# Kernel optimization log

Measured on AMD Instinct MI355X. Metric: run time of the kernel, lower is better.

## Reference

```python
import jax, jax.numpy as jnp
import numpy as np

B, NUM_GENES, F = 8, 20000, 128
N, E, H = 50000, 800000, 128


def setup_inputs() -> dict:
    key = jax.random.key(0)
    k = jax.random.split(key, 8)
    gene_emb = jax.random.normal(k[0], (B, NUM_GENES, F), dtype=jnp.float32)
    W1 = jax.random.normal(k[1], (F, H), dtype=jnp.float32) * 0.05
    b1 = jnp.zeros((H,), dtype=jnp.float32)
    W2 = jax.random.normal(k[2], (H, H), dtype=jnp.float32) * 0.05
    b2 = jnp.zeros((H,), dtype=jnp.float32)
    global_ids = jax.random.randint(k[3], (N,), 0, NUM_GENES, dtype=jnp.int64)
    edge_index = jax.random.randint(k[4], (2, E), 0, N, dtype=jnp.int64)
    return {"gene_emb": gene_emb, "W1": W1, "b1": b1, "W2": W2, "b2": b2,
            "global_ids": global_ids, "edge_index": edge_index}


def reference(gene_emb, W1, b1, W2, b2, global_ids, edge_index):
    n = global_ids.shape[0]
    # GCN normalization with self-loops (PyG GCNConv default):
    # A_hat = A + I, deg over target nodes, norm = d^{-1/2}[src] * d^{-1/2}[dst]
    loop = jnp.arange(n)
    src = jnp.concatenate([edge_index[0], loop])  # [E+N]
    dst = jnp.concatenate([edge_index[1], loop])  # [E+N]
    deg = jnp.zeros((n,), gene_emb.dtype).at[dst].add(1.0)
    dinv = jax.lax.rsqrt(deg)  # deg >= 1 thanks to self-loops
    norm = (dinv[src] * dinv[dst])[None, :, None]  # [1, E+N, 1]

    def gcn(x, W, b):
        h = x @ W                                   # [B, N, H] transform first (linear commutes)
        msg = h[:, src, :] * norm                   # gather + scale: [B, E+N, H]
        agg = jnp.zeros_like(h).at[:, dst].add(msg)  # scatter-add over targets
        return agg + b

    x = gene_emb[:, global_ids, :]                  # [B, N, F] node feature gather
    x = jax.nn.relu(gcn(x, W1, b1))
    x = gcn(x, W2, b2)
    # global_mean_pool: each batch replica is one whole graph -> mean over nodes
    return x.mean(axis=1)                           # [B, H]
```

## Files before the change

kernel.cpp:

```cpp
#include <hip/hip_runtime.h>

#define NG 20000
#define BB 8
#define FD 128

typedef unsigned int uint;
typedef unsigned short ushort;
typedef __attribute__((ext_vector_type(8))) short short8v;
typedef __attribute__((ext_vector_type(4))) float float4v;


__global__ void k_init(float* deg, float* s_acc, int N) {
    int i = blockIdx.x * blockDim.x + threadIdx.x;
    if (i < N) deg[i] = 1.0f;
    if (i < BB * FD) s_acc[i] = 0.0f;
}

__global__ void k_zero(int4* p, int n4) {
    int i = blockIdx.x * blockDim.x + threadIdx.x;
    if (i < n4) p[i] = make_int4(0, 0, 0, 0);
}

__global__ void k_count(const int* __restrict__ dst, float* deg, int E) {
    int e = blockIdx.x * blockDim.x + threadIdx.x;
    if (e < E) atomicAdd(&deg[dst[e]], 1.0f);
}

__global__ void k_node(const float* __restrict__ deg, float* dinv, float* cval,
                       float* wself, int* padcnt, int N) {
    int i = blockIdx.x * blockDim.x + threadIdx.x;
    if (i < N) {
        float d = deg[i];
        dinv[i]  = rsqrtf(d);
        float iv = 1.0f / d;
        cval[i]  = iv;
        wself[i] = iv;
        int nv = (int)d;
        padcnt[i] = (nv + 7) & ~7;
    }
}

__global__ void k_scan1(const int* __restrict__ padcnt, int* offs, int* bsums, int N) {
    __shared__ int sd[256];
    int t = threadIdx.x, idx = blockIdx.x * 256 + t;
    int v = (idx < N) ? padcnt[idx] : 0;
    sd[t] = v; __syncthreads();
    for (int o = 1; o < 256; o <<= 1) {
        int x = (t >= o) ? sd[t - o] : 0;
        __syncthreads();
        sd[t] += x;
        __syncthreads();
    }
    if (idx < N) offs[idx] = sd[t] - v;
    if (t == 255) bsums[blockIdx.x] = sd[255];
}

__global__ void k_scan2(int* bsums, int nb) {
    __shared__ int sd[256];
    int t = threadIdx.x;
    int v = (t < nb) ? bsums[t] : 0;
    sd[t] = v; __syncthreads();
    for (int o = 1; o < 256; o <<= 1) {
        int x = (t >= o) ? sd[t - o] : 0;
        __syncthreads();
        sd[t] += x;
        __syncthreads();
    }
    if (t < nb) bsums[t] = sd[t] - v;
}

__global__ void k_scan3(int* offs, const int* __restrict__ bsums, int N) {
    int i = blockIdx.x * blockDim.x + threadIdx.x;
    if (i < N) offs[i] += bsums[blockIdx.x];
}

__global__ void k_self(const int* __restrict__ gid, const float* __restrict__ wself,
                       const int* __restrict__ offs, int* cursor, int2* csr, int N) {
    int i = blockIdx.x * blockDim.x + threadIdx.x;
    if (i < N) {
        csr[offs[i]] = make_int2(gid[i], __float_as_int(wself[i]));
        cursor[i] = 1;
    }
}

__global__ void k_fill(const int* __restrict__ src, const int* __restrict__ dst,
                       const int* __restrict__ gid, const float* __restrict__ dinv,
                       float* cval, const int* __restrict__ offs, int* cursor,
                       int2* csr, int E) {
    int e = blockIdx.x * blockDim.x + threadIdx.x;
    if (e >= E) return;
    int s = src[e], d = dst[e];
    float nrm = dinv[s] * dinv[d];
    atomicAdd(&cval[s], nrm);
    int pos = atomicAdd(&cursor[d], 1);
    csr[offs[d] + pos] = make_int2(gid[s], __float_as_int(nrm));
}

__device__ __forceinline__ ushort f2bf(float x) {
    uint u = __float_as_uint(x);
    u += 0x7FFFu + ((u >> 16) & 1u);
    return (ushort)(u >> 16);
}
__device__ __forceinline__ float bf_lo(uint u) { return __uint_as_float(u << 16); }
__device__ __forceinline__ float bf_hi(uint u) { return __uint_as_float(u & 0xFFFF0000u); }

__global__ void k_w1t(const float* __restrict__ W1, ushort* __restrict__ w1t) {
    int j = blockIdx.x, k = threadIdx.x;
    w1t[j * 128 + k] = f2bf(W1[k * 128 + j]);
}

__global__ __launch_bounds__(256, 3)
void k_h(const float* __restrict__ gene, const ushort* __restrict__ w1t,
         ushort* __restrict__ h2) {
    __shared__ ushort Al[64 * 128];
    __shared__ ushort Bl[128 * 128];
    int t = threadIdx.x;
    size_t row0 = (size_t)blockIdx.x * 64;

#pragma unroll
    for (int s = 0; s < 8; s++) {
        int f = t + s * 256;
        int r = f >> 5, k0 = (f & 31) * 4;
        float4 v = *(const float4*)(gene + (row0 + r) * 128 + k0);
        ushort4 u;
        u.x = f2bf(v.x); u.y = f2bf(v.y); u.z = f2bf(v.z); u.w = f2bf(v.w);
        int byte = (r * 256 + k0 * 2) ^ ((r & 7) << 4);
        *(ushort4*)((char*)Al + byte) = u;
    }
#pragma unroll
    for (int s = 0; s < 8; s++) {
        int f = t + s * 256;
        int j = f >> 4, k0 = (f & 15) * 8;
        uint4 v = *(const uint4*)(w1t + j * 128 + k0);
        int byte = (j * 256 + k0 * 2) ^ ((j & 7) << 4);
        *(uint4*)((char*)Bl + byte) = v;
    }
    __syncthreads();

    int wid = t >> 6, lane = t & 63;
    int r0 = wid * 16;
    int lrow = lane & 15, lhi = lane >> 4;
    float4v acc[8];
#pragma unroll
    for (int nf = 0; nf < 8; nf++) acc[nf] = (float4v)(0.f);

#pragma unroll
    for (int c = 0; c < 4; c++) {
        int ra = r0 + lrow;
        int byteA = (ra * 256 + (c * 32 + lhi * 8) * 2) ^ ((ra & 7) << 4);
        short8v a = *(short8v*)((char*)Al + byteA);
#pragma unroll
        for (int nf = 0; nf < 8; nf++) {
            int jb = nf * 16 + lrow;
            int byteB = (jb * 256 + (c * 32 + lhi * 8) * 2) ^ ((jb & 7) << 4);
            short8v b = *(short8v*)((char*)Bl + byteB);
            acc[nf] = __builtin_amdgcn_mfma_f32_16x16x32_bf16(a, b, acc[nf], 0, 0, 0);
        }
    }
#pragma unroll
    for (int nf = 0; nf < 8; nf++) {
#pragma unroll
        for (int q = 0; q < 4; q++) {
            int rr = lhi * 4 + q;
            int cc = nf * 16 + lrow;
            h2[(row0 + r0 + rr) * 128 + cc] = f2bf(acc[nf][q]);
        }
    }
}

__global__ __launch_bounds__(512)
void k_aggs(const uint* __restrict__ hb, const int2* __restrict__ csr,
            const int* __restrict__ offs, const int* __restrict__ padcnt,
            const float* __restrict__ cval, const float* __restrict__ b1,
            float* __restrict__ s_acc, int N, int npw) {
    int b    = blockIdx.x & 7;
    int wid  = threadIdx.x >> 6, lane = threadIdx.x & 63;
    int w    = __builtin_amdgcn_readfirstlane((blockIdx.x >> 3) * 8 + wid);
    const uint* base = hb + (size_t)b * NG * 64;
    int j = lane * 2;
    float bx = b1[j], by = b1[j + 1];
    float sx = 0.f, sy = 0.f;

    int i0 = w * npw;
    int i1 = min(N, i0 + npw);
    for (int i = i0; i < i1; ++i) {
        int   e  = offs[i];
        int   pc = padcnt[i];
        float cv = cval[i];
        float ax = 0.f, ay = 0.f;
        for (int q = 0; q < pc; q += 8) {
            int ee = e + q;
            int2 c0 = csr[ee],     c1 = csr[ee + 1], c2 = csr[ee + 2], c3 = csr[ee + 3];
            int2 c4 = csr[ee + 4], c5 = csr[ee + 5], c6 = csr[ee + 6], c7 = csr[ee + 7];
            uint u0 = base[(size_t)c0.x * 64 + lane];
            uint u1 = base[(size_t)c1.x * 64 + lane];
            uint u2 = base[(size_t)c2.x * 64 + lane];
            uint u3 = base[(size_t)c3.x * 64 + lane];
            uint u4 = base[(size_t)c4.x * 64 + lane];
            uint u5 = base[(size_t)c5.x * 64 + lane];
            uint u6 = base[(size_t)c6.x * 64 + lane];
            uint u7 = base[(size_t)c7.x * 64 + lane];
            float n0 = __int_as_float(c0.y), n1 = __int_as_float(c1.y);
            float n2 = __int_as_float(c2.y), n3 = __int_as_float(c3.y);
            float n4 = __int_as_float(c4.y), n5 = __int_as_float(c5.y);
            float n6 = __int_as_float(c6.y), n7 = __int_as_float(c7.y);
            ax = fmaf(n0, bf_lo(u0), ax); ay = fmaf(n0, bf_hi(u0), ay);
            ax = fmaf(n1, bf_lo(u1), ax); ay = fmaf(n1, bf_hi(u1), ay);
            ax = fmaf(n2, bf_lo(u2), ax); ay = fmaf(n2, bf_hi(u2), ay);
            ax = fmaf(n3, bf_lo(u3), ax); ay = fmaf(n3, bf_hi(u3), ay);
            ax = fmaf(n4, bf_lo(u4), ax); ay = fmaf(n4, bf_hi(u4), ay);
            ax = fmaf(n5, bf_lo(u5), ax); ay = fmaf(n5, bf_hi(u5), ay);
            ax = fmaf(n6, bf_lo(u6), ax); ay = fmaf(n6, bf_hi(u6), ay);
            ax = fmaf(n7, bf_lo(u7), ax); ay = fmaf(n7, bf_hi(u7), ay);
        }
        sx += cv * fmaxf(ax + bx, 0.f);
        sy += cv * fmaxf(ay + by, 0.f);
    }

    __shared__ float red[8][128];
    red[wid][j]     = sx;
    red[wid][j + 1] = sy;
    __syncthreads();
    int t = threadIdx.x;
    if (t < 128) {
        float s = 0.f;
#pragma unroll
        for (int wv = 0; wv < 8; wv++) s += red[wv][t];
        atomicAdd(&s_acc[b * 128 + t], s);
    }
}

__global__ void k_final(const float* __restrict__ s_acc, const float* __restrict__ W2,
                        const float* __restrict__ b2, float* __restrict__ out, float invN) {
    __shared__ float ss[1024];
    int t = threadIdx.x;
    for (int idx = t; idx < 1024; idx += 128) ss[idx] = s_acc[idx];
    __syncthreads();
    float acc[8];
#pragma unroll
    for (int b = 0; b < 8; b++) acc[b] = 0.f;
    for (int k = 0; k < 128; k++) {
        float w = W2[k * 128 + t];
#pragma unroll
        for (int b = 0; b < 8; b++) acc[b] += ss[b * 128 + k] * w;
    }
    float bb = b2[t];
#pragma unroll
    for (int b = 0; b < 8; b++) out[b * 128 + t] = acc[b] * invN + bb;
}


extern "C" void kernel_launch(void* const* d_in, const int* in_sizes, int n_in,
                              void* d_out, int out_size, void* d_ws, size_t ws_size,
                              hipStream_t stream) {
    const float* gene = (const float*)d_in[0];
    const float* W1   = (const float*)d_in[1];
    const float* b1   = (const float*)d_in[2];
    const float* W2   = (const float*)d_in[3];
    const float* b2   = (const float*)d_in[4];
    const int*   gid  = (const int*)d_in[5];
    const int*   eidx = (const int*)d_in[6];
    int N = in_sizes[5];
    int E = in_sizes[6] / 2;
    const int* src = eidx;
    const int* dst = eidx + E;
    float* out = (float*)d_out;

    char* p = (char*)d_ws;
    auto alloc = [&](size_t bytes) -> char* {
        char* r = p; p += (bytes + 255) & ~(size_t)255; return r;
    };
    size_t csr_cap = (size_t)E + 8 * (size_t)N;
    float* deg    = (float*)alloc((size_t)N * 4);
    float* dinv   = (float*)alloc((size_t)N * 4);
    float* cval   = (float*)alloc((size_t)N * 4);
    float* wself  = (float*)alloc((size_t)N * 4);
    int*   padcnt = (int*)  alloc((size_t)N * 4);
    int*   offs   = (int*)  alloc((size_t)N * 4);
    int*   cursor = (int*)  alloc((size_t)N * 4);
    int*   bsums  = (int*)  alloc(256 * 4);
    int2*  csr    = (int2*) alloc(csr_cap * 8);
    float* s_acc  = (float*)alloc(1024 * 4);
    ushort* h2    = (ushort*)alloc((size_t)NG * BB * FD * 2);
    ushort* w1t   = (ushort*)alloc(128 * 128 * 2);

    int nb = (N + 255) / 256;
    int eb = (E + 255) / 256;
    int zn4 = (int)(csr_cap * 8 / 16);
    int zb  = (zn4 + 255) / 256;

    const int NBLK = 2048;
    int wavesPerBatch = (NBLK / 8) * 8;
    int npw = (N + wavesPerBatch - 1) / wavesPerBatch;

    k_init <<<nb, 256, 0, stream>>>(deg, s_acc, N);
    k_zero <<<zb, 256, 0, stream>>>((int4*)csr, zn4);
    k_w1t  <<<128, 128, 0, stream>>>(W1, w1t);
    k_count<<<eb, 256, 0, stream>>>(dst, deg, E);
    k_node <<<nb, 256, 0, stream>>>(deg, dinv, cval, wself, padcnt, N);
    k_scan1<<<nb, 256, 0, stream>>>(padcnt, offs, bsums, N);
    k_scan2<<<1, 256, 0, stream>>>(bsums, nb);
    k_scan3<<<nb, 256, 0, stream>>>(offs, bsums, N);
    k_self <<<nb, 256, 0, stream>>>(gid, wself, offs, cursor, csr, N);
    k_fill <<<eb, 256, 0, stream>>>(src, dst, gid, dinv, cval, offs, cursor, csr, E);
    k_h    <<<(NG * BB) / 64, 256, 0, stream>>>(gene, w1t, h2);
    k_aggs <<<NBLK, 512, 0, stream>>>((const uint*)h2, csr, offs, padcnt,
                                      cval, b1, s_acc, N, npw);
    k_final<<<1, 128, 0, stream>>>(s_acc, W2, b2, out, 1.0f / (float)N);
}
```

Baseline: 332.7 us.

## Interleave batch pairs in the hidden layout and fuse setup/scan kernels

The bf16 hidden features are now stored with two batch replicas interleaved per feature. This lets the aggregation kernel gather 8 bytes per lane covering two batches at once, so each CSR edge read is shared across two batches and the number of CSR passes halves. Several small preprocessing kernels (init, zero, W1 transpose, node stats, scan stages, self-loop fill) are merged into fewer launches to cut launch overhead. Each wave now does twice the work per node and holds more accumulator registers.

```diff
diff --git a/kernel.cpp b/kernel.cpp
--- a/kernel.cpp
+++ b/kernel.cpp
@@ -9,16 +9,24 @@
 typedef __attribute__((ext_vector_type(8))) short short8v;
 typedef __attribute__((ext_vector_type(4))) float float4v;
 
-
-__global__ void k_init(float* deg, float* s_acc, int N) {
+__device__ __forceinline__ ushort f2bf(float x) {
+    uint u = __float_as_uint(x);
+    u += 0x7FFFu + ((u >> 16) & 1u);
+    return (ushort)(u >> 16);
+}
+__device__ __forceinline__ float bf_lo(uint u) { return __uint_as_float(u << 16); }
+__device__ __forceinline__ float bf_hi(uint u) { return __uint_as_float(u & 0xFFFF0000u); }
+
+__global__ void k_setup(int4* csrz, int zn4, float* deg, float* s_acc,
+                        const float* __restrict__ W1, ushort* w1t, int N) {
     int i = blockIdx.x * blockDim.x + threadIdx.x;
+    if (i < zn4) csrz[i] = make_int4(0, 0, 0, 0);
     if (i < N) deg[i] = 1.0f;
     if (i < BB * FD) s_acc[i] = 0.0f;
-}
-
-__global__ void k_zero(int4* p, int n4) {
-    int i = blockIdx.x * blockDim.x + threadIdx.x;
-    if (i < n4) p[i] = make_int4(0, 0, 0, 0);
+    if (i < FD * FD) {
+        int j = i >> 7, k = i & 127;
+        w1t[i] = f2bf(W1[k * 128 + j]);
+    }
 }
 
 __global__ void k_count(const int* __restrict__ dst, float* deg, int E) {
@@ -26,24 +34,20 @@
     if (e < E) atomicAdd(&deg[dst[e]], 1.0f);
 }
 
-__global__ void k_node(const float* __restrict__ deg, float* dinv, float* cval,
-                       float* wself, int* padcnt, int N) {
-    int i = blockIdx.x * blockDim.x + threadIdx.x;
-    if (i < N) {
-        float d = deg[i];
-        dinv[i]  = rsqrtf(d);
-        float iv = 1.0f / d;
-        cval[i]  = iv;
-        wself[i] = iv;
-        int nv = (int)d;
-        padcnt[i] = (nv + 7) & ~7;
-    }
-}
-
-__global__ void k_scan1(const int* __restrict__ padcnt, int* offs, int* bsums, int N) {
+__global__ void k_scanA(const float* __restrict__ deg, float* dinv, float* cval,
+                        float* wself, int* padcnt, int* offs, int* bsums, int N) {
     __shared__ int sd[256];
     int t = threadIdx.x, idx = blockIdx.x * 256 + t;
-    int v = (idx < N) ? padcnt[idx] : 0;
+    int v = 0;
+    if (idx < N) {
+        float d = deg[idx];
+        dinv[idx]  = rsqrtf(d);
+        float iv = 1.0f / d;
+        cval[idx]  = iv;
+        wself[idx] = iv;
+        v = ((int)d + 7) & ~7;
+        padcnt[idx] = v;
+    }
     sd[t] = v; __syncthreads();
     for (int o = 1; o < 256; o <<= 1) {
         int x = (t >= o) ? sd[t - o] : 0;
@@ -69,16 +73,14 @@
     if (t < nb) bsums[t] = sd[t] - v;
 }
 
-__global__ void k_scan3(int* offs, const int* __restrict__ bsums, int N) {
-    int i = blockIdx.x * blockDim.x + threadIdx.x;
-    if (i < N) offs[i] += bsums[blockIdx.x];
-}
-
-__global__ void k_self(const int* __restrict__ gid, const float* __restrict__ wself,
-                       const int* __restrict__ offs, int* cursor, int2* csr, int N) {
+__global__ void k_scanB(int* offs, const int* __restrict__ bsums,
+                        const int* __restrict__ gid, const float* __restrict__ wself,
+                        int* cursor, int2* csr, int N) {
     int i = blockIdx.x * blockDim.x + threadIdx.x;
     if (i < N) {
-        csr[offs[i]] = make_int2(gid[i], __float_as_int(wself[i]));
+        int o = offs[i] + bsums[blockIdx.x];
+        offs[i] = o;
+        csr[o] = make_int2(gid[i], __float_as_int(wself[i]));
         cursor[i] = 1;
     }
 }
@@ -96,19 +98,6 @@
     csr[offs[d] + pos] = make_int2(gid[s], __float_as_int(nrm));
 }
 
-__device__ __forceinline__ ushort f2bf(float x) {
-    uint u = __float_as_uint(x);
-    u += 0x7FFFu + ((u >> 16) & 1u);
-    return (ushort)(u >> 16);
-}
-__device__ __forceinline__ float bf_lo(uint u) { return __uint_as_float(u << 16); }
-__device__ __forceinline__ float bf_hi(uint u) { return __uint_as_float(u & 0xFFFF0000u); }
-
-__global__ void k_w1t(const float* __restrict__ W1, ushort* __restrict__ w1t) {
-    int j = blockIdx.x, k = threadIdx.x;
-    w1t[j * 128 + k] = f2bf(W1[k * 128 + j]);
-}
-
 __global__ __launch_bounds__(256, 3)
 void k_h(const float* __restrict__ gene, const ushort* __restrict__ w1t,
          ushort* __restrict__ h2) {
@@ -163,23 +152,27 @@
         for (int q = 0; q < 4; q++) {
             int rr = lhi * 4 + q;
             int cc = nf * 16 + lrow;
-            h2[(row0 + r0 + rr) * 128 + cc] = f2bf(acc[nf][q]);
+            int rGlob = (int)row0 + r0 + rr;
+            int bb = rGlob / NG;
+            int gg = rGlob - bb * NG;
+            size_t di = ((size_t)(bb >> 1) * NG + gg) * 256 + cc * 2 + (bb & 1);
+            h2[di] = f2bf(acc[nf][q]);
         }
     }
 }
 
 __global__ __launch_bounds__(512)
-void k_aggs(const uint* __restrict__ hb, const int2* __restrict__ csr,
+void k_aggp(const uint* __restrict__ hp, const int2* __restrict__ csr,
             const int* __restrict__ offs, const int* __restrict__ padcnt,
             const float* __restrict__ cval, const float* __restrict__ b1,
             float* __restrict__ s_acc, int N, int npw) {
-    int b    = blockIdx.x & 7;
+    int p    = blockIdx.x & 3;
     int wid  = threadIdx.x >> 6, lane = threadIdx.x & 63;
-    int w    = __builtin_amdgcn_readfirstlane((blockIdx.x >> 3) * 8 + wid);
-    const uint* base = hb + (size_t)b * NG * 64;
-    int j = lane * 2;
-    float bx = b1[j], by = b1[j + 1];
-    float sx = 0.f, sy = 0.f;
+    int w    = __builtin_amdgcn_readfirstlane((blockIdx.x >> 2) * 8 + wid);
+    const uint* bp = hp + (size_t)p * NG * 128 + lane * 2;
+    int l2 = lane * 2;
+    float bx = b1[l2], by = b1[l2 + 1];
+    float sx0 = 0.f, sx1 = 0.f, sy0 = 0.f, sy1 = 0.f;
 
     int i0 = w * npw;
     int i1 = min(N, i0 + npw);
@@ -187,46 +180,59 @@
         int   e  = offs[i];
         int   pc = padcnt[i];
         float cv = cval[i];
-        float ax = 0.f, ay = 0.f;
+        float ax0 = 0.f, ax1 = 0.f, ay0 = 0.f, ay1 = 0.f;
         for (int q = 0; q < pc; q += 8) {
             int ee = e + q;
             int2 c0 = csr[ee],     c1 = csr[ee + 1], c2 = csr[ee + 2], c3 = csr[ee + 3];
             int2 c4 = csr[ee + 4], c5 = csr[ee + 5], c6 = csr[ee + 6], c7 = csr[ee + 7];
-            uint u0 = base[(size_t)c0.x * 64 + lane];
-            uint u1 = base[(size_t)c1.x * 64 + lane];
-            uint u2 = base[(size_t)c2.x * 64 + lane];
-            uint u3 = base[(size_t)c3.x * 64 + lane];
-            uint u4 = base[(size_t)c4.x * 64 + lane];
-            uint u5 = base[(size_t)c5.x * 64 + lane];
-            uint u6 = base[(size_t)c6.x * 64 + lane];
-            uint u7 = base[(size_t)c7.x * 64 + lane];
+            uint2 u0 = *(const uint2*)(bp + (size_t)c0.x * 128);
+            uint2 u1 = *(const uint2*)(bp + (size_t)c1.x * 128);
+            uint2 u2 = *(const uint2*)(bp + (size_t)c2.x * 128);
+            uint2 u3 = *(const uint2*)(bp + (size_t)c3.x * 128);
+            uint2 u4 = *(const uint2*)(bp + (size_t)c4.x * 128);
+            uint2 u5 = *(const uint2*)(bp + (size_t)c5.x * 128);
+            uint2 u6 = *(const uint2*)(bp + (size_t)c6.x * 128);
+            uint2 u7 = *(const uint2*)(bp + (size_t)c7.x * 128);
             float n0 = __int_as_float(c0.y), n1 = __int_as_float(c1.y);
             float n2 = __int_as_float(c2.y), n3 = __int_as_float(c3.y);
             float n4 = __int_as_float(c4.y), n5 = __int_as_float(c5.y);
             float n6 = __int_as_float(c6.y), n7 = __int_as_float(c7.y);
-            ax = fmaf(n0, bf_lo(u0), ax); ay = fmaf(n0, bf_hi(u0), ay);
-            ax = fmaf(n1, bf_lo(u1), ax); ay = fmaf(n1, bf_hi(u1), ay);
-            ax = fmaf(n2, bf_lo(u2), ax); ay = fmaf(n2, bf_hi(u2), ay);
-            ax = fmaf(n3, bf_lo(u3), ax); ay = fmaf(n3, bf_hi(u3), ay);
-            ax = fmaf(n4, bf_lo(u4), ax); ay = fmaf(n4, bf_hi(u4), ay);
-            ax = fmaf(n5, bf_lo(u5), ax); ay = fmaf(n5, bf_hi(u5), ay);
-            ax = fmaf(n6, bf_lo(u6), ax); ay = fmaf(n6, bf_hi(u6), ay);
-            ax = fmaf(n7, bf_lo(u7), ax); ay = fmaf(n7, bf_hi(u7), ay);
+            ax0 = fmaf(n0, bf_lo(u0.x), ax0); ax1 = fmaf(n0, bf_hi(u0.x), ax1);
+            ay0 = fmaf(n0, bf_lo(u0.y), ay0); ay1 = fmaf(n0, bf_hi(u0.y), ay1);
+            ax0 = fmaf(n1, bf_lo(u1.x), ax0); ax1 = fmaf(n1, bf_hi(u1.x), ax1);
+            ay0 = fmaf(n1, bf_lo(u1.y), ay0); ay1 = fmaf(n1, bf_hi(u1.y), ay1);
+            ax0 = fmaf(n2, bf_lo(u2.x), ax0); ax1 = fmaf(n2, bf_hi(u2.x), ax1);
+            ay0 = fmaf(n2, bf_lo(u2.y), ay0); ay1 = fmaf(n2, bf_hi(u2.y), ay1);
+            ax0 = fmaf(n3, bf_lo(u3.x), ax0); ax1 = fmaf(n3, bf_hi(u3.x), ax1);
+            ay0 = fmaf(n3, bf_lo(u3.y), ay0); ay1 = fmaf(n3, bf_hi(u3.y), ay1);
+            ax0 = fmaf(n4, bf_lo(u4.x), ax0); ax1 = fmaf(n4, bf_hi(u4.x), ax1);
+            ay0 = fmaf(n4, bf_lo(u4.y), ay0); ay1 = fmaf(n4, bf_hi(u4.y), ay1);
+            ax0 = fmaf(n5, bf_lo(u5.x), ax0); ax1 = fmaf(n5, bf_hi(u5.x), ax1);
+            ay0 = fmaf(n5, bf_lo(u5.y), ay0); ay1 = fmaf(n5, bf_hi(u5.y), ay1);
+            ax0 = fmaf(n6, bf_lo(u6.x), ax0); ax1 = fmaf(n6, bf_hi(u6.x), ax1);
+            ay0 = fmaf(n6, bf_lo(u6.y), ay0); ay1 = fmaf(n6, bf_hi(u6.y), ay1);
+            ax0 = fmaf(n7, bf_lo(u7.x), ax0); ax1 = fmaf(n7, bf_hi(u7.x), ax1);
+            ay0 = fmaf(n7, bf_lo(u7.y), ay0); ay1 = fmaf(n7, bf_hi(u7.y), ay1);
         }
-        sx += cv * fmaxf(ax + bx, 0.f);
-        sy += cv * fmaxf(ay + by, 0.f);
-    }
-
-    __shared__ float red[8][128];
-    red[wid][j]     = sx;
-    red[wid][j + 1] = sy;
+        sx0 += cv * fmaxf(ax0 + bx, 0.f);
+        sx1 += cv * fmaxf(ax1 + bx, 0.f);
+        sy0 += cv * fmaxf(ay0 + by, 0.f);
+        sy1 += cv * fmaxf(ay1 + by, 0.f);
+    }
+
+    __shared__ float red[8][256];
+    red[wid][lane * 4 + 0] = sx0;
+    red[wid][lane * 4 + 1] = sx1;
+    red[wid][lane * 4 + 2] = sy0;
+    red[wid][lane * 4 + 3] = sy1;
     __syncthreads();
     int t = threadIdx.x;
-    if (t < 128) {
+    if (t < 256) {
         float s = 0.f;
 #pragma unroll
         for (int wv = 0; wv < 8; wv++) s += red[wv][t];
-        atomicAdd(&s_acc[b * 128 + t], s);
+        int l = t >> 2, c = t & 3;
+        atomicAdd(&s_acc[(2 * p + (c & 1)) * 128 + 2 * l + (c >> 1)], s);
     }
 }
 
@@ -290,21 +296,17 @@
     int zb  = (zn4 + 255) / 256;
 
     const int NBLK = 2048;
-    int wavesPerBatch = (NBLK / 8) * 8;
-    int npw = (N + wavesPerBatch - 1) / wavesPerBatch;
-
-    k_init <<<nb, 256, 0, stream>>>(deg, s_acc, N);
-    k_zero <<<zb, 256, 0, stream>>>((int4*)csr, zn4);
-    k_w1t  <<<128, 128, 0, stream>>>(W1, w1t);
+    int wavesPerPair = (NBLK / 4) * 8;
+    int npw = (N + wavesPerPair - 1) / wavesPerPair;
+
+    k_setup<<<zb, 256, 0, stream>>>((int4*)csr, zn4, deg, s_acc, W1, w1t, N);
     k_count<<<eb, 256, 0, stream>>>(dst, deg, E);
-    k_node <<<nb, 256, 0, stream>>>(deg, dinv, cval, wself, padcnt, N);
-    k_scan1<<<nb, 256, 0, stream>>>(padcnt, offs, bsums, N);
+    k_scanA<<<nb, 256, 0, stream>>>(deg, dinv, cval, wself, padcnt, offs, bsums, N);
     k_scan2<<<1, 256, 0, stream>>>(bsums, nb);
-    k_scan3<<<nb, 256, 0, stream>>>(offs, bsums, N);
-    k_self <<<nb, 256, 0, stream>>>(gid, wself, offs, cursor, csr, N);
+    k_scanB<<<nb, 256, 0, stream>>>(offs, bsums, gid, wself, cursor, csr, N);
     k_fill <<<eb, 256, 0, stream>>>(src, dst, gid, dinv, cval, offs, cursor, csr, E);
     k_h    <<<(NG * BB) / 64, 256, 0, stream>>>(gene, w1t, h2);
-    k_aggs <<<NBLK, 512, 0, stream>>>((const uint*)h2, csr, offs, padcnt,
+    k_aggp <<<NBLK, 512, 0, stream>>>((const uint*)h2, csr, offs, padcnt,
                                       cval, b1, s_acc, N, npw);
     k_final<<<1, 128, 0, stream>>>(s_acc, W2, b2, out, 1.0f / (float)N);
 }
```

Measured after the change: 331.3 us. No clear change (-0.4%).
